# Optimization experiments

Measured on AMD Instinct MI355X. Metric: run time of the kernel, lower is better.

Reference implementation:

```python
import jax, jax.numpy as jnp
import numpy as np

N = 8192
E = 262144
D_IN = 256
D_OUT = 256
EPS = 1e-05


def setup_inputs() -> dict:
    key = jax.random.key(0)
    kx, ke0, ke1, kw = jax.random.split(key, 4)
    x = jax.random.normal(kx, (N, D_IN), dtype=jnp.float32)
    edge_index = jnp.stack([
        jax.random.randint(ke0, (E,), 0, N, dtype=jnp.int64),
        jax.random.randint(ke1, (E,), 0, N, dtype=jnp.int64),
    ], axis=0)
    # nn.Linear(in, out, bias=False): weight shape [out, in], kaiming-uniform-ish init
    bound = 1.0 / np.sqrt(D_IN)
    W = jax.random.uniform(kw, (D_OUT, D_IN), dtype=jnp.float32, minval=-bound, maxval=bound)
    return {"x": x, "edge_index": edge_index, "W": W}


def reference(x, edge_index, W):
    n = x.shape[0]
    # A_hat = I with edges set to 1 (set semantics; duplicates harmless)
    A_hat = jnp.eye(n, dtype=x.dtype).at[edge_index[0], edge_index[1]].set(1.0)
    # D_hat = diag(1/sqrt(rowsum + eps)); A_norm = D_hat @ A_hat @ D_hat
    d_inv = 1.0 / jnp.sqrt(A_hat.sum(axis=1) + EPS)  # [N]
    A_norm = d_inv[:, None] * A_hat * d_inv[None, :]  # [N, N]
    h = x @ W.T  # [N, D_OUT]
    return jax.nn.relu(A_norm @ h)
```

## Files before the change

kernel.cpp:

```cpp
#include <hip/hip_runtime.h>
#include <hip/hip_bf16.h>
#include <math.h>

#define N_NODES 8192
#define DIM 256
#define WPR 256
#define MAXN 1024

typedef __attribute__((ext_vector_type(8))) short bf16x8;
typedef __attribute__((ext_vector_type(4))) float f32x4;

__global__ __launch_bounds__(256) void scatter_edges(const int* __restrict__ rows,
                                                     const int* __restrict__ cols,
                                                     unsigned* __restrict__ bitmap, int E) {
    int e = blockIdx.x * 256 + threadIdx.x;
    if (e >= E) return;
    int r = rows[e];
    int c = cols[e];
    atomicOr(&bitmap[(size_t)r * WPR + (c >> 5)], 1u << (c & 31));
}

__global__ __launch_bounds__(256) void compute_dinv(const unsigned* __restrict__ bitmap,
                                                    float* __restrict__ dinv) {
    int wave = threadIdx.x >> 6;
    int lane = threadIdx.x & 63;
    int row = blockIdx.x * 4 + wave;
    const uint4* base = (const uint4*)(bitmap + (size_t)row * WPR);
    uint4 w = base[lane];
    int cnt = __popc(w.x) + __popc(w.y) + __popc(w.z) + __popc(w.w);
    int dw = row >> 5;
    int diag = 0;
    if ((dw >> 2) == lane) {
        unsigned word = ((dw & 3) == 0) ? w.x : ((dw & 3) == 1) ? w.y : ((dw & 3) == 2) ? w.z : w.w;
        diag = (int)((word >> (row & 31)) & 1u);
    }
#pragma unroll
    for (int off = 32; off > 0; off >>= 1) cnt += __shfl_down(cnt, off);
    int diag_any = (__ballot(diag) != 0ull) ? 1 : 0;
    if (lane == 0) {
        float rowsum = (float)(cnt + (diag_any ? 0 : 1));
        dinv[row] = 1.0f / sqrtf(rowsum + 1e-5f);
    }
}

__global__ __launch_bounds__(256) void convert_bf16(const float* __restrict__ x,
                                                    const float* __restrict__ W,
                                                    __hip_bfloat16* __restrict__ xb,
                                                    __hip_bfloat16* __restrict__ Wb) {
    size_t i4 = ((size_t)blockIdx.x * 256 + threadIdx.x) * 4;
    const size_t NX = (size_t)N_NODES * DIM;
    const float* src;
    __hip_bfloat16* dst;
    size_t off;
    if (i4 < NX) { src = x; dst = xb; off = i4; }
    else         { src = W; dst = Wb; off = i4 - NX; }
    float4 v = *(const float4*)(src + off);
    union { __hip_bfloat16 h[4]; uint2 u; } t;
    t.h[0] = __float2bfloat16(v.x);
    t.h[1] = __float2bfloat16(v.y);
    t.h[2] = __float2bfloat16(v.z);
    t.h[3] = __float2bfloat16(v.w);
    *(uint2*)(dst + off) = t.u;
}

__global__ __launch_bounds__(256) void gemm_mfma(const short* __restrict__ xb,
                                                 const short* __restrict__ Wb,
                                                 const float* __restrict__ dinv,
                                                 __hip_bfloat16* __restrict__ g) {
    int wave = threadIdx.x >> 6;
    int lane = threadIdx.x & 63;
    int bm = blockIdx.x * 64 + wave * 16;
    int bn = blockIdx.y * 64;
    int quad = lane >> 4;
    int l16 = lane & 15;
    f32x4 acc[4] = {};
    const short* arow = xb + (size_t)(bm + l16) * DIM + quad * 8;
#pragma unroll
    for (int k0 = 0; k0 < DIM; k0 += 32) {
        bf16x8 a = *(const bf16x8*)(arow + k0);
#pragma unroll
        for (int s = 0; s < 4; s++) {
            bf16x8 b = *(const bf16x8*)(Wb + (size_t)(bn + s * 16 + l16) * DIM + k0 + quad * 8);
            acc[s] = __builtin_amdgcn_mfma_f32_16x16x32_bf16(a, b, acc[s], 0, 0, 0);
        }
    }
#pragma unroll
    for (int r = 0; r < 4; r++) {
        int m = bm + quad * 4 + r;
        float s0 = dinv[m];
#pragma unroll
        for (int s = 0; s < 4; s++)
            g[(size_t)m * DIM + bn + s * 16 + l16] = __float2bfloat16(s0 * acc[s][r]);
    }
}

__global__ __launch_bounds__(128) void aggregate(const unsigned* __restrict__ bitmap,
                                                 const unsigned* __restrict__ g32,
                                                 const float* __restrict__ dinv,
                                                 float* __restrict__ out) {
    __shared__ int nbr[MAXN];
    __shared__ int cnt;
    int row = blockIdx.x;
    int tid = threadIdx.x;
    if (tid == 0) cnt = 0;
    __syncthreads();
    uint2 wv = *(const uint2*)(bitmap + (size_t)row * WPR + tid * 2);
#pragma unroll
    for (int half = 0; half < 2; half++) {
        unsigned w = (half == 0) ? wv.x : wv.y;
        int base = tid * 64 + half * 32;
        while (w) {
            int b = __builtin_ctz(w);
            w &= w - 1;
            nbr[atomicAdd(&cnt, 1)] = base + b;
        }
    }
    if (tid == 0) {
        unsigned dwv = bitmap[(size_t)row * WPR + (row >> 5)];
        if (!((dwv >> (row & 31)) & 1u)) nbr[atomicAdd(&cnt, 1)] = row;
    }
    __syncthreads();
    int n = cnt;
    float2 a0 = {0.f, 0.f}, a1 = {0.f, 0.f}, a2 = {0.f, 0.f}, a3 = {0.f, 0.f};
    int i = 0;
    for (; i + 4 <= n; i += 4) {
        unsigned u0 = g32[(size_t)nbr[i + 0] * 128 + tid];
        unsigned u1 = g32[(size_t)nbr[i + 1] * 128 + tid];
        unsigned u2 = g32[(size_t)nbr[i + 2] * 128 + tid];
        unsigned u3 = g32[(size_t)nbr[i + 3] * 128 + tid];
        a0.x += __uint_as_float(u0 << 16); a0.y += __uint_as_float(u0 & 0xffff0000u);
        a1.x += __uint_as_float(u1 << 16); a1.y += __uint_as_float(u1 & 0xffff0000u);
        a2.x += __uint_as_float(u2 << 16); a2.y += __uint_as_float(u2 & 0xffff0000u);
        a3.x += __uint_as_float(u3 << 16); a3.y += __uint_as_float(u3 & 0xffff0000u);
    }
    for (; i < n; i++) {
        unsigned u = g32[(size_t)nbr[i] * 128 + tid];
        a0.x += __uint_as_float(u << 16); a0.y += __uint_as_float(u & 0xffff0000u);
    }
    float s = dinv[row];
    float2 o;
    o.x = fmaxf(s * ((a0.x + a1.x) + (a2.x + a3.x)), 0.f);
    o.y = fmaxf(s * ((a0.y + a1.y) + (a2.y + a3.y)), 0.f);
    *(float2*)(out + (size_t)row * DIM + tid * 2) = o;
}

extern "C" void kernel_launch(void* const* d_in, const int* in_sizes, int n_in,
                              void* d_out, int out_size, void* d_ws, size_t ws_size,
                              hipStream_t stream) {
    const float* x = (const float*)d_in[0];
    const int* ei = (const int*)d_in[1];
    const float* W = (const float*)d_in[2];
    float* out = (float*)d_out;
    int E = in_sizes[1] / 2;

    unsigned char* ws = (unsigned char*)d_ws;
    size_t off = 0;
    unsigned* bitmap = (unsigned*)(ws + off); off += (size_t)N_NODES * WPR * 4;
    float* dinv = (float*)(ws + off);        off += (size_t)N_NODES * 4;
    __hip_bfloat16* xb = (__hip_bfloat16*)(ws + off); off += (size_t)N_NODES * DIM * 2;
    __hip_bfloat16* Wb = (__hip_bfloat16*)(ws + off); off += (size_t)DIM * DIM * 2;
    __hip_bfloat16* g = (__hip_bfloat16*)(ws + off);  off += (size_t)N_NODES * DIM * 2;

    hipMemsetAsync(bitmap, 0, (size_t)N_NODES * WPR * 4, stream);
    scatter_edges<<<(E + 255) / 256, 256, 0, stream>>>(ei, ei + E, bitmap, E);
    compute_dinv<<<N_NODES / 4, 256, 0, stream>>>(bitmap, dinv);
    int conv_threads = (N_NODES * DIM + DIM * DIM) / 4;
    convert_bf16<<<conv_threads / 256, 256, 0, stream>>>(x, W, xb, Wb);
    dim3 ggrid(N_NODES / 64, DIM / 64);
    gemm_mfma<<<ggrid, 256, 0, stream>>>((const short*)xb, (const short*)Wb, dinv, g);
    aggregate<<<N_NODES, 128, 0, stream>>>(bitmap, (const unsigned*)g, dinv, out);
}
```

Baseline: 107.5 us.

## Build per-row neighbor lists during edge scatter and drop dinv kernel

```diff
diff --git a/kernel.cpp b/kernel.cpp
--- a/kernel.cpp
+++ b/kernel.cpp
@@ -5,41 +5,42 @@
 #define N_NODES 8192
 #define DIM 256
 #define WPR 256
-#define MAXN 1024
+#define MAXD 128
+#define EPS 1e-5f
 
 typedef __attribute__((ext_vector_type(8))) short bf16x8;
 typedef __attribute__((ext_vector_type(4))) float f32x4;
 
-__global__ __launch_bounds__(256) void scatter_edges(const int* __restrict__ rows,
-                                                     const int* __restrict__ cols,
-                                                     unsigned* __restrict__ bitmap, int E) {
+__global__ __launch_bounds__(256) void init_ds(unsigned* __restrict__ bitmap,
+                                               int* __restrict__ degree,
+                                               int* __restrict__ cols) {
+    int t = blockIdx.x * 256 + threadIdx.x;
+    int w0 = t * 4;
+    int row = w0 >> 8;
+    int rel = w0 & 255;
+    int diagw = row >> 5;
+    union { unsigned w[4]; uint4 v; } u;
+    u.v = make_uint4(0, 0, 0, 0);
+    if (diagw >= rel && diagw < rel + 4)
+        u.w[diagw - rel] = 1u << (row & 31);
+    ((uint4*)bitmap)[t] = u.v;
+    if (rel == 0) { degree[row] = 1; cols[(size_t)row * MAXD] = row; }
+}
+
+__global__ __launch_bounds__(256) void scatter_edges(const int* __restrict__ erows,
+                                                     const int* __restrict__ ecols,
+                                                     unsigned* __restrict__ bitmap,
+                                                     int* __restrict__ degree,
+                                                     int* __restrict__ cols, int E) {
     int e = blockIdx.x * 256 + threadIdx.x;
     if (e >= E) return;
-    int r = rows[e];
-    int c = cols[e];
-    atomicOr(&bitmap[(size_t)r * WPR + (c >> 5)], 1u << (c & 31));
-}
-
-__global__ __launch_bounds__(256) void compute_dinv(const unsigned* __restrict__ bitmap,
-                                                    float* __restrict__ dinv) {
-    int wave = threadIdx.x >> 6;
-    int lane = threadIdx.x & 63;
-    int row = blockIdx.x * 4 + wave;
-    const uint4* base = (const uint4*)(bitmap + (size_t)row * WPR);
-    uint4 w = base[lane];
-    int cnt = __popc(w.x) + __popc(w.y) + __popc(w.z) + __popc(w.w);
-    int dw = row >> 5;
-    int diag = 0;
-    if ((dw >> 2) == lane) {
-        unsigned word = ((dw & 3) == 0) ? w.x : ((dw & 3) == 1) ? w.y : ((dw & 3) == 2) ? w.z : w.w;
-        diag = (int)((word >> (row & 31)) & 1u);
-    }
-#pragma unroll
-    for (int off = 32; off > 0; off >>= 1) cnt += __shfl_down(cnt, off);
-    int diag_any = (__ballot(diag) != 0ull) ? 1 : 0;
-    if (lane == 0) {
-        float rowsum = (float)(cnt + (diag_any ? 0 : 1));
-        dinv[row] = 1.0f / sqrtf(rowsum + 1e-5f);
+    int r = erows[e];
+    int c = ecols[e];
+    unsigned bit = 1u << (c & 31);
+    unsigned old = atomicOr(&bitmap[(size_t)r * WPR + (c >> 5)], bit);
+    if (!(old & bit)) {
+        int p = atomicAdd(&degree[r], 1);
+        cols[(size_t)r * MAXD + p] = c;
     }
 }
 
@@ -65,7 +66,7 @@
 
 __global__ __launch_bounds__(256) void gemm_mfma(const short* __restrict__ xb,
                                                  const short* __restrict__ Wb,
-                                                 const float* __restrict__ dinv,
+                                                 const int* __restrict__ degree,
                                                  __hip_bfloat16* __restrict__ g) {
     int wave = threadIdx.x >> 6;
     int lane = threadIdx.x & 63;
@@ -87,61 +88,54 @@
 #pragma unroll
     for (int r = 0; r < 4; r++) {
         int m = bm + quad * 4 + r;
-        float s0 = dinv[m];
+        float s0 = rsqrtf((float)degree[m] + EPS);
 #pragma unroll
         for (int s = 0; s < 4; s++)
             g[(size_t)m * DIM + bn + s * 16 + l16] = __float2bfloat16(s0 * acc[s][r]);
     }
 }
 
-__global__ __launch_bounds__(128) void aggregate(const unsigned* __restrict__ bitmap,
-                                                 const unsigned* __restrict__ g32,
-                                                 const float* __restrict__ dinv,
+__global__ __launch_bounds__(256) void aggregate(const int* __restrict__ degree,
+                                                 const int* __restrict__ cols,
+                                                 const uint2* __restrict__ g2,
                                                  float* __restrict__ out) {
-    __shared__ int nbr[MAXN];
-    __shared__ int cnt;
-    int row = blockIdx.x;
-    int tid = threadIdx.x;
-    if (tid == 0) cnt = 0;
-    __syncthreads();
-    uint2 wv = *(const uint2*)(bitmap + (size_t)row * WPR + tid * 2);
-#pragma unroll
-    for (int half = 0; half < 2; half++) {
-        unsigned w = (half == 0) ? wv.x : wv.y;
-        int base = tid * 64 + half * 32;
-        while (w) {
-            int b = __builtin_ctz(w);
-            w &= w - 1;
-            nbr[atomicAdd(&cnt, 1)] = base + b;
-        }
-    }
-    if (tid == 0) {
-        unsigned dwv = bitmap[(size_t)row * WPR + (row >> 5)];
-        if (!((dwv >> (row & 31)) & 1u)) nbr[atomicAdd(&cnt, 1)] = row;
-    }
-    __syncthreads();
-    int n = cnt;
-    float2 a0 = {0.f, 0.f}, a1 = {0.f, 0.f}, a2 = {0.f, 0.f}, a3 = {0.f, 0.f};
+    int wave = threadIdx.x >> 6;
+    int lane = threadIdx.x & 63;
+    int row = blockIdx.x * 4 + wave;
+    int n = degree[row];
+    const int* cl = cols + (size_t)row * MAXD;
+    float a0[4] = {0.f, 0.f, 0.f, 0.f};
+    float a1[4] = {0.f, 0.f, 0.f, 0.f};
+    float a2[4] = {0.f, 0.f, 0.f, 0.f};
+    float a3[4] = {0.f, 0.f, 0.f, 0.f};
     int i = 0;
     for (; i + 4 <= n; i += 4) {
-        unsigned u0 = g32[(size_t)nbr[i + 0] * 128 + tid];
-        unsigned u1 = g32[(size_t)nbr[i + 1] * 128 + tid];
-        unsigned u2 = g32[(size_t)nbr[i + 2] * 128 + tid];
-        unsigned u3 = g32[(size_t)nbr[i + 3] * 128 + tid];
-        a0.x += __uint_as_float(u0 << 16); a0.y += __uint_as_float(u0 & 0xffff0000u);
-        a1.x += __uint_as_float(u1 << 16); a1.y += __uint_as_float(u1 & 0xffff0000u);
-        a2.x += __uint_as_float(u2 << 16); a2.y += __uint_as_float(u2 & 0xffff0000u);
-        a3.x += __uint_as_float(u3 << 16); a3.y += __uint_as_float(u3 & 0xffff0000u);
+        int j0 = cl[i], j1 = cl[i + 1], j2 = cl[i + 2], j3 = cl[i + 3];
+        uint2 u0 = g2[(size_t)j0 * 64 + lane];
+        uint2 u1 = g2[(size_t)j1 * 64 + lane];
+        uint2 u2 = g2[(size_t)j2 * 64 + lane];
+        uint2 u3 = g2[(size_t)j3 * 64 + lane];
+        a0[0] += __uint_as_float(u0.x << 16); a0[1] += __uint_as_float(u0.x & 0xffff0000u);
+        a0[2] += __uint_as_float(u0.y << 16); a0[3] += __uint_as_float(u0.y & 0xffff0000u);
+        a1[0] += __uint_as_float(u1.x << 16); a1[1] += __uint_as_float(u1.x & 0xffff0000u);
+        a1[2] += __uint_as_float(u1.y << 16); a1[3] += __uint_as_float(u1.y & 0xffff0000u);
+        a2[0] += __uint_as_float(u2.x << 16); a2[1] += __uint_as_float(u2.x & 0xffff0000u);
+        a2[2] += __uint_as_float(u2.y << 16); a2[3] += __uint_as_float(u2.y & 0xffff0000u);
+        a3[0] += __uint_as_float(u3.x << 16); a3[1] += __uint_as_float(u3.x & 0xffff0000u);
+        a3[2] += __uint_as_float(u3.y << 16); a3[3] += __uint_as_float(u3.y & 0xffff0000u);
     }
     for (; i < n; i++) {
-        unsigned u = g32[(size_t)nbr[i] * 128 + tid];
-        a0.x += __uint_as_float(u << 16); a0.y += __uint_as_float(u & 0xffff0000u);
+        uint2 u = g2[(size_t)cl[i] * 64 + lane];
+        a0[0] += __uint_as_float(u.x << 16); a0[1] += __uint_as_float(u.x & 0xffff0000u);
+        a0[2] += __uint_as_float(u.y << 16); a0[3] += __uint_as_float(u.y & 0xffff0000u);
     }
-    float s = dinv[row];
-    float2 o;
-    o.x = fmaxf(s * ((a0.x + a1.x) + (a2.x + a3.x)), 0.f);
-    o.y = fmaxf(s * ((a0.y + a1.y) + (a2.y + a3.y)), 0.f);
-    *(float2*)(out + (size_t)row * DIM + tid * 2) = o;
+    float s = rsqrtf((float)n + EPS);
+    float4 o;
+    o.x = fmaxf(s * ((a0[0] + a1[0]) + (a2[0] + a3[0])), 0.f);
+    o.y = fmaxf(s * ((a0[1] + a1[1]) + (a2[1] + a3[1])), 0.f);
+    o.z = fmaxf(s * ((a0[2] + a1[2]) + (a2[2] + a3[2])), 0.f);
+    o.w = fmaxf(s * ((a0[3] + a1[3]) + (a2[3] + a3[3])), 0.f);
+    *(float4*)(out + (size_t)row * DIM + lane * 4) = o;
 }
 
 extern "C" void kernel_launch(void* const* d_in, const int* in_sizes, int n_in,
@@ -156,17 +150,17 @@
     unsigned char* ws = (unsigned char*)d_ws;
     size_t off = 0;
     unsigned* bitmap = (unsigned*)(ws + off); off += (size_t)N_NODES * WPR * 4;
-    float* dinv = (float*)(ws + off);        off += (size_t)N_NODES * 4;
+    int* degree = (int*)(ws + off);           off += (size_t)N_NODES * 4;
+    int* cols = (int*)(ws + off);             off += (size_t)N_NODES * MAXD * 4;
     __hip_bfloat16* xb = (__hip_bfloat16*)(ws + off); off += (size_t)N_NODES * DIM * 2;
     __hip_bfloat16* Wb = (__hip_bfloat16*)(ws + off); off += (size_t)DIM * DIM * 2;
     __hip_bfloat16* g = (__hip_bfloat16*)(ws + off);  off += (size_t)N_NODES * DIM * 2;
 
-    hipMemsetAsync(bitmap, 0, (size_t)N_NODES * WPR * 4, stream);
-    scatter_edges<<<(E + 255) / 256, 256, 0, stream>>>(ei, ei + E, bitmap, E);
-    compute_dinv<<<N_NODES / 4, 256, 0, stream>>>(bitmap, dinv);
+    init_ds<<<N_NODES * WPR / 4 / 256, 256, 0, stream>>>(bitmap, degree, cols);
+    scatter_edges<<<(E + 255) / 256, 256, 0, stream>>>(ei, ei + E, bitmap, degree, cols, E);
     int conv_threads = (N_NODES * DIM + DIM * DIM) / 4;
     convert_bf16<<<conv_threads / 256, 256, 0, stream>>>(x, W, xb, Wb);
     dim3 ggrid(N_NODES / 64, DIM / 64);
-    gemm_mfma<<<ggrid, 256, 0, stream>>>((const short*)xb, (const short*)Wb, dinv, g);
-    aggregate<<<N_NODES, 128, 0, stream>>>(bitmap, (const unsigned*)g, dinv, out);
+    gemm_mfma<<<ggrid, 256, 0, stream>>>((const short*)xb, (const short*)Wb, degree, g);
+    aggregate<<<N_NODES / 4, 256, 0, stream>>>(degree, cols, (const uint2*)g, out);
 }
```

Measured after the change: 132.3 us. +23.1%, slower.
